# Kernel optimization log

Measured on AMD Instinct MI355X. Metric: run time of the kernel, lower is better.

The kernel has to match this reference:

```python
import jax, jax.numpy as jnp
from jax import lax
import numpy as np

WIDTH = 3.0        # tool half-width (voxels)
SIGMA = 1.0        # soft mask edge (voxels)
BLUR_SIGMA = 1.5   # post-deposit isotropic blur sigma (voxels)
EPS = 1e-8


def _gauss_blur(x, sigma):
    """Separable Gaussian blur over the last two axes of x: [B, X, Y]."""
    radius = int(3 * sigma)
    t = jnp.arange(-radius, radius + 1, dtype=x.dtype)
    k = jnp.exp(-0.5 * (t / sigma) ** 2)
    k = k / k.sum()
    x4 = x[:, None]                      # [B,1,X,Y] NCHW
    kh = k.reshape(1, 1, -1, 1)
    x4 = lax.conv_general_dilated(x4, kh, (1, 1), 'SAME')
    kw = k.reshape(1, 1, 1, -1)
    x4 = lax.conv_general_dilated(x4, kw, (1, 1), 'SAME')
    return x4[:, 0]


def setup_inputs() -> dict:
    key = jax.random.key(0)
    k1, k2, k3 = jax.random.split(key, 3)
    B, H, W = 16, 1024, 1024
    occ = jax.random.uniform(k1, (B, H, W), dtype=jnp.float32)
    # push start/end points well inside the grid (voxel coordinates)
    action_start = jax.random.uniform(k2, (B, 3), minval=200.0, maxval=800.0, dtype=jnp.float32)
    action_end = action_start + jax.random.uniform(k3, (B, 3), minval=-150.0, maxval=150.0, dtype=jnp.float32)
    return {"occ": occ, "action_start": action_start, "action_end": action_end}


def reference(occ, action_start, action_end):
    # coordinate-convention transpose (see SplatPushModel docs)
    rho = jnp.swapaxes(occ, 1, 2)            # [B, X, Y]
    B, X, Y = rho.shape
    p0 = action_start[:, :2]                 # [B,2]
    p1 = action_end[:, :2]                   # [B,2]

    d = p1 - p0
    L = jnp.sqrt(jnp.sum(d * d, axis=-1) + EPS)      # [B] segment length
    u = d / L[:, None]                               # unit push direction
    n = jnp.stack([-u[:, 1], u[:, 0]], axis=-1)      # unit normal

    gx = jnp.arange(X, dtype=rho.dtype)[None, :, None]   # [1,X,1]
    gy = jnp.arange(Y, dtype=rho.dtype)[None, None, :]   # [1,1,Y]
    bc = lambda v: v[:, None, None]                      # [B] -> [B,1,1]

    # --- swept band: soft distance-to-segment mask ---
    rx = gx - bc(p0[:, 0])
    ry = gy - bc(p0[:, 1])
    t = jnp.clip(rx * bc(u[:, 0]) + ry * bc(u[:, 1]), 0.0, L[:, None, None])
    dx = rx - t * bc(u[:, 0])
    dy = ry - t * bc(u[:, 1])
    dist = jnp.sqrt(dx * dx + dy * dy + EPS)
    swept = jax.nn.sigmoid((WIDTH - dist) / SIGMA)       # [B,X,Y]

    m_swept = jnp.sum(rho * swept, axis=(1, 2))          # [B] mass to move
    pile_depth = m_swept / (2.0 * WIDTH)                 # [B]

    # --- landing zone probe (rectangle past p1) ---
    qx = gx - bc(p1[:, 0])
    qy = gy - bc(p1[:, 1])
    s = qx * bc(u[:, 0]) + qy * bc(u[:, 1])              # along-direction coord
    r = qx * bc(n[:, 0]) + qy * bc(n[:, 1])              # perpendicular coord
    lat = jax.nn.sigmoid((WIDTH - jnp.abs(r)) / SIGMA)
    probe = jax.nn.sigmoid(s / SIGMA) * jax.nn.sigmoid((bc(pile_depth) - s) / SIGMA) * lat
    existing = jnp.sum(rho * probe, axis=(1, 2))         # [B]
    extra = existing / (2.0 * WIDTH)                     # [B] forward extension

    # --- deposit band, shifted forward by extra_depth ---
    dep_mask = (jax.nn.sigmoid((s - bc(extra)) / SIGMA)
                * jax.nn.sigmoid((bc(extra) + bc(pile_depth) - s) / SIGMA)
                * lat)
    dep_norm = m_swept / (jnp.sum(dep_mask, axis=(1, 2)) + EPS)
    dep = dep_mask * dep_norm[:, None, None]             # mass-conserving deposit

    if BLUR_SIGMA > 0:
        dep = _gauss_blur(dep, BLUR_SIGMA)

    rho_new = rho * (1.0 - swept) + dep
    return jnp.swapaxes(rho_new, 1, 2)
```

## Files before the change

kernel.cpp:

```cpp
#include <hip/hip_runtime.h>
#include <hip/hip_bf16.h>
#include <math.h>

#define BB    16
#define HH    1024
#define WW    1024
#define NPIX  (HH * WW)
#define EPSF  1e-8f
#define RAD   4
#define MARG  24.f
#define NBX   128
#define NPATCH 64

struct BlurK { float k[9]; };

__device__ __forceinline__ float sigf(float z) {
    z = fmaxf(fminf(z, 40.f), -40.f);
    return 1.f / (1.f + __expf(-z));
}

struct Geom { float p0x, p0y, p1x, p1y, L, ux, uy; };

__device__ __forceinline__ Geom load_geom(const float* as, const float* ae, int b) {
    Geom g;
    g.p0x = as[3 * b];  g.p0y = as[3 * b + 1];
    g.p1x = ae[3 * b];  g.p1y = ae[3 * b + 1];
    float dx = g.p1x - g.p0x, dy = g.p1y - g.p0y;
    g.L  = sqrtf(dx * dx + dy * dy + EPSF);
    g.ux = dx / g.L;  g.uy = dy / g.L;
    return g;
}

__device__ __forceinline__ float sweptf(const Geom& g, float x, float y) {
    float rx = x - g.p0x, ry = y - g.p0y;
    float t  = fminf(fmaxf(rx * g.ux + ry * g.uy, 0.f), g.L);
    float dx = rx - t * g.ux, dy = ry - t * g.uy;
    float dist = sqrtf(dx * dx + dy * dy + EPSF);
    return sigf(3.f - dist);
}

__device__ __forceinline__ void slat(const Geom& g, float x, float y, float& s, float& lat) {
    float qx = x - g.p1x, qy = y - g.p1y;
    s = qx * g.ux + qy * g.uy;
    float r = qx * (-g.uy) + qy * g.ux;
    lat = sigf(3.f - fabsf(r));
}

__device__ __forceinline__ void capsule_bbox(const Geom& g, float m,
                                             int& x0, int& x1, int& y0, int& y1) {
    x0 = max(0, (int)floorf(fminf(g.p0x, g.p1x) - m));
    x1 = min(WW - 1, (int)ceilf(fmaxf(g.p0x, g.p1x) + m));
    y0 = max(0, (int)floorf(fminf(g.p0y, g.p1y) - m));
    y1 = min(HH - 1, (int)ceilf(fmaxf(g.p0y, g.p1y) + m));
}

__device__ __forceinline__ void strip_bbox(const Geom& g, float s0, float s1, float m,
                                           int& x0, int& x1, int& y0, int& y1) {
    float xmin = 1e9f, xmax = -1e9f, ymin = 1e9f, ymax = -1e9f;
    #pragma unroll
    for (int i = 0; i < 4; i++) {
        float s = (i & 1) ? s1 : s0;
        float r = (i & 2) ? m : -m;
        float x = g.p1x + s * g.ux - r * g.uy;
        float y = g.p1y + s * g.uy + r * g.ux;
        xmin = fminf(xmin, x); xmax = fmaxf(xmax, x);
        ymin = fminf(ymin, y); ymax = fmaxf(ymax, y);
    }
    x0 = max(0, (int)floorf(xmin)); x1 = min(WW - 1, (int)ceilf(xmax));
    y0 = max(0, (int)floorf(ymin)); y1 = min(HH - 1, (int)ceilf(ymax));
}

__device__ __forceinline__ float brb256(float v, float* sm) {
    #pragma unroll
    for (int off = 32; off > 0; off >>= 1) v += __shfl_down(v, off);
    const int lane = threadIdx.x & 63, wid = threadIdx.x >> 6;
    if (lane == 0) sm[wid] = v;
    __syncthreads();
    float r = sm[0] + sm[1] + sm[2] + sm[3];
    __syncthreads();
    return r;
}

__global__ __launch_bounds__(256)
void k_phase1(const float* __restrict__ occ, const float* __restrict__ as,
              const float* __restrict__ ae, float* __restrict__ out,
              float* __restrict__ part1) {
    const int b = blockIdx.y, bx = blockIdx.x, tid = threadIdx.x;
    const float4* src = (const float4*)(occ + ((size_t)b << 20));
    float4*       dst = (float4*)(out + ((size_t)b << 20));
    const int cb = bx * 1024 + tid;
    float4 v0 = src[cb];
    float4 v1 = src[cb + 256];
    float4 v2 = src[cb + 512];
    float4 v3 = src[cb + 768];

    Geom g = load_geom(as, ae, b);
    int x0, x1, y0, y1; capsule_bbox(g, MARG, x0, x1, y0, y1);
    const float* base = occ + ((size_t)b << 20);
    float sum = 0.f;
    for (int y = y0 + bx; y <= y1; y += NBX) {
        float fy = (float)y;
        for (int x = x0 + tid; x <= x1; x += 256)
            sum += base[((size_t)y << 10) + x] * sweptf(g, (float)x, fy);
    }

    dst[cb] = v0; dst[cb + 256] = v1; dst[cb + 512] = v2; dst[cb + 768] = v3;

    __shared__ float sm[4];
    float bs = brb256(sum, sm);
    if (tid == 0) part1[b * NBX + bx] = bs;
}

__global__ __launch_bounds__(256)
void k_phase2(const float* __restrict__ occ, const float* __restrict__ as,
              const float* __restrict__ ae, float* __restrict__ out,
              const float* __restrict__ part1, float* __restrict__ part2) {
    const int b = blockIdx.y, bx = blockIdx.x, tid = threadIdx.x;
    const float4* src = (const float4*)(occ + ((size_t)b << 20));
    float4*       dst = (float4*)(out + ((size_t)b << 20));
    const int cb = 131072 + bx * 1024 + tid;
    float4 v0 = src[cb];
    float4 v1 = src[cb + 256];
    float4 v2 = src[cb + 512];
    float4 v3 = src[cb + 768];

    __shared__ float sm[4];
    float pv = (tid < NBX) ? part1[b * NBX + tid] : 0.f;
    const float m_swept = brb256(pv, sm);
    const float pile = m_swept * (1.f / 6.f);

    Geom g = load_geom(as, ae, b);
    int x0, x1, y0, y1; strip_bbox(g, -MARG, pile + MARG, MARG, x0, x1, y0, y1);
    const float* base = occ + ((size_t)b << 20);
    float sum = 0.f;
    for (int y = y0 + bx; y <= y1; y += NBX) {
        float fy = (float)y;
        for (int x = x0 + tid; x <= x1; x += 256) {
            float s, lat; slat(g, (float)x, fy, s, lat);
            sum += base[((size_t)y << 10) + x] * sigf(s) * sigf(pile - s) * lat;
        }
    }

    dst[cb] = v0; dst[cb + 256] = v1; dst[cb + 512] = v2; dst[cb + 768] = v3;

    float bs = brb256(sum, sm);
    if (tid == 0) part2[b * NBX + bx] = bs;
}

#define TH 8
#define TW 128
__global__ __launch_bounds__(256)
void k_final(const float* __restrict__ occ, const float* __restrict__ as,
             const float* __restrict__ ae, const float* __restrict__ part1,
             const float* __restrict__ part2, float* __restrict__ out, BlurK wk) {
    const int b = blockIdx.y, bx = blockIdx.x, tid = threadIdx.x;
    __shared__ float sm[4];
    Geom g = load_geom(as, ae, b);

    const float m_swept  = brb256((tid < NBX) ? part1[b * NBX + tid] : 0.f, sm);
    const float existing = brb256((tid < NBX) ? part2[b * NBX + tid] : 0.f, sm);
    const float pile  = m_swept * (1.f / 6.f);
    const float extra = existing * (1.f / 6.f);

    int sx0, sx1, sy0, sy1;
    strip_bbox(g, extra - MARG, extra + pile + MARG, MARG, sx0, sx1, sy0, sy1);
    float sum = 0.f;
    {
        const int w = sx1 - sx0 + 1, n = w * (sy1 - sy0 + 1);
        for (int i = tid; i < n; i += 256) {
            int y = sy0 + i / w, x = sx0 + i % w;
            float s, lat; slat(g, (float)x, (float)y, s, lat);
            sum += sigf(s - extra) * sigf(extra + pile - s) * lat;
        }
    }
    const float summask = brb256(sum, sm);
    const float dep_norm = m_swept / (summask + EPSF);

    int cx0, cx1, cy0, cy1; capsule_bbox(g, MARG, cx0, cx1, cy0, cy1);
    const int ux0 = min(cx0, sx0), ux1 = max(cx1, sx1);
    const int uy0 = min(cy0, sy0), uy1 = max(cy1, sy1);
    const int bw = ux1 - ux0 + 1, bh = uy1 - uy0 + 1;
    const int ntx = (bw + TW - 1) / TW, nty = (bh + TH - 1) / TH;

    __shared__ float draw[TH + 2 * RAD][TW + 2 * RAD];
    __shared__ float hb[TH + 2 * RAD][TW];
    const float* ob = occ + ((size_t)b << 20);
    float* outb = out + ((size_t)b << 20);

    for (int t = bx; t < ntx * nty; t += NPATCH) {
        const int tx = t % ntx, ty = t / ntx;
        const int xt = ux0 + tx * TW, yt = uy0 + ty * TH;
        for (int i = tid; i < (TH + 8) * (TW + 8); i += 256) {
            int ly = i / (TW + 8), lx = i % (TW + 8);
            int gy = yt - RAD + ly, gx = xt - RAD + lx;
            float v = 0.f;
            if (gx >= 0 && gx < WW && gy >= 0 && gy < HH) {
                float s, lat; slat(g, (float)gx, (float)gy, s, lat);
                v = sigf(s - extra) * sigf(extra + pile - s) * lat * dep_norm;
            }
            draw[ly][lx] = v;
        }
        __syncthreads();
        for (int i = tid; i < (TH + 8) * TW; i += 256) {
            int ly = i / TW, lx = i % TW;
            float acc = 0.f;
            #pragma unroll
            for (int j = 0; j < 9; j++) acc += wk.k[j] * draw[ly][lx + j];
            hb[ly][lx] = acc;
        }
        __syncthreads();
        for (int i = tid; i < TH * TW; i += 256) {
            int ly = i / TW, lx = i % TW;
            int gy = yt + ly, gx = xt + lx;
            if (gy < HH && gx < WW) {
                float acc = 0.f;
                #pragma unroll
                for (int j = 0; j < 9; j++) acc += wk.k[j] * hb[ly + j][lx];
                size_t off = ((size_t)gy << 10) + gx;
                float o = ob[off];
                outb[off] = o * (1.f - sweptf(g, (float)gx, (float)gy)) + acc;
            }
        }
        __syncthreads();
    }
}

extern "C" void kernel_launch(void* const* d_in, const int* in_sizes, int n_in,
                              void* d_out, int out_size, void* d_ws, size_t ws_size,
                              hipStream_t stream) {
    const float* occ = (const float*)d_in[0];
    const float* as  = (const float*)d_in[1];
    const float* ae  = (const float*)d_in[2];
    float* out   = (float*)d_out;
    float* part1 = (float*)d_ws;
    float* part2 = (float*)d_ws + BB * NBX;

    BlurK wk;
    {
        float s = 0.f;
        for (int i = 0; i < 9; i++) {
            float t = (float)(i - RAD) / 1.5f;
            wk.k[i] = expf(-0.5f * t * t);
            s += wk.k[i];
        }
        for (int i = 0; i < 9; i++) wk.k[i] /= s;
    }

    k_phase1<<<dim3(NBX, BB),    256, 0, stream>>>(occ, as, ae, out, part1);
    k_phase2<<<dim3(NBX, BB),    256, 0, stream>>>(occ, as, ae, out, part1, part2);
    k_final <<<dim3(NPATCH, BB), 256, 0, stream>>>(occ, as, ae, part1, part2, out, wk);
}
```

Baseline: 165.4 us.

## Fuse full copy into first pass, reuse copied data for swept sum, split summask kernel

The first kernel now copies the whole 4 MB image per batch itself, eight float4 rows per thread, and computes the swept-mass sum from those registers. This removes the second strided global read over the capsule bbox. The existing-mass kernel no longer copies and runs with 64 blocks. The deposit-mask normalisation sum moves out of the final kernel into its own grid-parallel kernel, so each patch block no longer repeats that full strip scan. This adds one more kernel launch, and the first kernel moves more bytes per block, which may lower occupancy.

```diff
diff --git a/kernel.cpp b/kernel.cpp
--- a/kernel.cpp
+++ b/kernel.cpp
@@ -9,8 +9,8 @@
 #define EPSF  1e-8f
 #define RAD   4
 #define MARG  24.f
-#define NBX   128
-#define NPATCH 64
+#define NB1   128
+#define NB2   64
 
 struct BlurK { float k[9]; };
 
@@ -82,101 +82,109 @@
 }
 
 __global__ __launch_bounds__(256)
-void k_phase1(const float* __restrict__ occ, const float* __restrict__ as,
-              const float* __restrict__ ae, float* __restrict__ out,
-              float* __restrict__ part1) {
+void k_copy_mswept(const float* __restrict__ occ, const float* __restrict__ as,
+                   const float* __restrict__ ae, float* __restrict__ out,
+                   float* __restrict__ part1) {
     const int b = blockIdx.y, bx = blockIdx.x, tid = threadIdx.x;
     const float4* src = (const float4*)(occ + ((size_t)b << 20));
     float4*       dst = (float4*)(out + ((size_t)b << 20));
-    const int cb = bx * 1024 + tid;
-    float4 v0 = src[cb];
-    float4 v1 = src[cb + 256];
-    float4 v2 = src[cb + 512];
-    float4 v3 = src[cb + 768];
-
-    Geom g = load_geom(as, ae, b);
-    int x0, x1, y0, y1; capsule_bbox(g, MARG, x0, x1, y0, y1);
-    const float* base = occ + ((size_t)b << 20);
+    const int base4 = bx * 2048 + tid;
+    float4 v[8];
+    #pragma unroll
+    for (int k = 0; k < 8; k++) v[k] = src[base4 + k * 256];
+    #pragma unroll
+    for (int k = 0; k < 8; k++) dst[base4 + k * 256] = v[k];
+
+    Geom g = load_geom(as, ae, b);
+    int cx0, cx1, cy0, cy1; capsule_bbox(g, MARG, cx0, cx1, cy0, cy1);
+    const int x = tid << 2;
     float sum = 0.f;
-    for (int y = y0 + bx; y <= y1; y += NBX) {
-        float fy = (float)y;
-        for (int x = x0 + tid; x <= x1; x += 256)
-            sum += base[((size_t)y << 10) + x] * sweptf(g, (float)x, fy);
-    }
-
-    dst[cb] = v0; dst[cb + 256] = v1; dst[cb + 512] = v2; dst[cb + 768] = v3;
-
+    if (x + 3 >= cx0 && x <= cx1) {
+        #pragma unroll
+        for (int k = 0; k < 8; k++) {
+            const int y = bx * 8 + k;
+            if (y >= cy0 && y <= cy1) {
+                float fy = (float)y, fx = (float)x;
+                sum += v[k].x * sweptf(g, fx + 0.f, fy);
+                sum += v[k].y * sweptf(g, fx + 1.f, fy);
+                sum += v[k].z * sweptf(g, fx + 2.f, fy);
+                sum += v[k].w * sweptf(g, fx + 3.f, fy);
+            }
+        }
+    }
     __shared__ float sm[4];
     float bs = brb256(sum, sm);
-    if (tid == 0) part1[b * NBX + bx] = bs;
-}
-
-__global__ __launch_bounds__(256)
-void k_phase2(const float* __restrict__ occ, const float* __restrict__ as,
-              const float* __restrict__ ae, float* __restrict__ out,
-              const float* __restrict__ part1, float* __restrict__ part2) {
-    const int b = blockIdx.y, bx = blockIdx.x, tid = threadIdx.x;
-    const float4* src = (const float4*)(occ + ((size_t)b << 20));
-    float4*       dst = (float4*)(out + ((size_t)b << 20));
-    const int cb = 131072 + bx * 1024 + tid;
-    float4 v0 = src[cb];
-    float4 v1 = src[cb + 256];
-    float4 v2 = src[cb + 512];
-    float4 v3 = src[cb + 768];
-
-    __shared__ float sm[4];
-    float pv = (tid < NBX) ? part1[b * NBX + tid] : 0.f;
-    const float m_swept = brb256(pv, sm);
+    if (tid == 0) part1[b * NB1 + bx] = bs;
+}
+
+__global__ __launch_bounds__(256)
+void k_existing(const float* __restrict__ occ, const float* __restrict__ as,
+                const float* __restrict__ ae, const float* __restrict__ part1,
+                float* __restrict__ part2) {
+    const int b = blockIdx.y, bx = blockIdx.x, tid = threadIdx.x;
+    __shared__ float sm[4];
+    const float m_swept = brb256((tid < NB1) ? part1[b * NB1 + tid] : 0.f, sm);
     const float pile = m_swept * (1.f / 6.f);
 
     Geom g = load_geom(as, ae, b);
     int x0, x1, y0, y1; strip_bbox(g, -MARG, pile + MARG, MARG, x0, x1, y0, y1);
     const float* base = occ + ((size_t)b << 20);
     float sum = 0.f;
-    for (int y = y0 + bx; y <= y1; y += NBX) {
+    for (int y = y0 + bx; y <= y1; y += NB2) {
         float fy = (float)y;
         for (int x = x0 + tid; x <= x1; x += 256) {
             float s, lat; slat(g, (float)x, fy, s, lat);
             sum += base[((size_t)y << 10) + x] * sigf(s) * sigf(pile - s) * lat;
         }
     }
-
-    dst[cb] = v0; dst[cb + 256] = v1; dst[cb + 512] = v2; dst[cb + 768] = v3;
-
     float bs = brb256(sum, sm);
-    if (tid == 0) part2[b * NBX + bx] = bs;
+    if (tid == 0) part2[b * NB2 + bx] = bs;
+}
+
+__global__ __launch_bounds__(256)
+void k_summask(const float* __restrict__ as, const float* __restrict__ ae,
+               const float* __restrict__ part1, const float* __restrict__ part2,
+               float* __restrict__ part3) {
+    const int b = blockIdx.y, bx = blockIdx.x, tid = threadIdx.x;
+    __shared__ float sm[4];
+    const float m_swept  = brb256((tid < NB1) ? part1[b * NB1 + tid] : 0.f, sm);
+    const float existing = brb256((tid < NB2) ? part2[b * NB2 + tid] : 0.f, sm);
+    const float pile  = m_swept * (1.f / 6.f);
+    const float extra = existing * (1.f / 6.f);
+
+    Geom g = load_geom(as, ae, b);
+    int x0, x1, y0, y1; strip_bbox(g, extra - MARG, extra + pile + MARG, MARG, x0, x1, y0, y1);
+    float sum = 0.f;
+    for (int y = y0 + bx; y <= y1; y += NB2) {
+        float fy = (float)y;
+        for (int x = x0 + tid; x <= x1; x += 256) {
+            float s, lat; slat(g, (float)x, fy, s, lat);
+            sum += sigf(s - extra) * sigf(extra + pile - s) * lat;
+        }
+    }
+    float bs = brb256(sum, sm);
+    if (tid == 0) part3[b * NB2 + bx] = bs;
 }
 
 #define TH 8
 #define TW 128
 __global__ __launch_bounds__(256)
-void k_final(const float* __restrict__ occ, const float* __restrict__ as,
+void k_patch(const float* __restrict__ occ, const float* __restrict__ as,
              const float* __restrict__ ae, const float* __restrict__ part1,
-             const float* __restrict__ part2, float* __restrict__ out, BlurK wk) {
-    const int b = blockIdx.y, bx = blockIdx.x, tid = threadIdx.x;
-    __shared__ float sm[4];
-    Geom g = load_geom(as, ae, b);
-
-    const float m_swept  = brb256((tid < NBX) ? part1[b * NBX + tid] : 0.f, sm);
-    const float existing = brb256((tid < NBX) ? part2[b * NBX + tid] : 0.f, sm);
-    const float pile  = m_swept * (1.f / 6.f);
-    const float extra = existing * (1.f / 6.f);
-
-    int sx0, sx1, sy0, sy1;
-    strip_bbox(g, extra - MARG, extra + pile + MARG, MARG, sx0, sx1, sy0, sy1);
-    float sum = 0.f;
-    {
-        const int w = sx1 - sx0 + 1, n = w * (sy1 - sy0 + 1);
-        for (int i = tid; i < n; i += 256) {
-            int y = sy0 + i / w, x = sx0 + i % w;
-            float s, lat; slat(g, (float)x, (float)y, s, lat);
-            sum += sigf(s - extra) * sigf(extra + pile - s) * lat;
-        }
-    }
-    const float summask = brb256(sum, sm);
+             const float* __restrict__ part2, const float* __restrict__ part3,
+             float* __restrict__ out, BlurK wk) {
+    const int b = blockIdx.y, bx = blockIdx.x, tid = threadIdx.x;
+    __shared__ float sm[4];
+    const float m_swept  = brb256((tid < NB1) ? part1[b * NB1 + tid] : 0.f, sm);
+    const float existing = brb256((tid < NB2) ? part2[b * NB2 + tid] : 0.f, sm);
+    const float summask  = brb256((tid < NB2) ? part3[b * NB2 + tid] : 0.f, sm);
+    const float pile     = m_swept * (1.f / 6.f);
+    const float extra    = existing * (1.f / 6.f);
     const float dep_norm = m_swept / (summask + EPSF);
 
+    Geom g = load_geom(as, ae, b);
     int cx0, cx1, cy0, cy1; capsule_bbox(g, MARG, cx0, cx1, cy0, cy1);
+    int sx0, sx1, sy0, sy1; strip_bbox(g, extra - MARG, extra + pile + MARG, MARG, sx0, sx1, sy0, sy1);
     const int ux0 = min(cx0, sx0), ux1 = max(cx1, sx1);
     const int uy0 = min(cy0, sy0), uy1 = max(cy1, sy1);
     const int bw = ux1 - ux0 + 1, bh = uy1 - uy0 + 1;
@@ -187,7 +195,7 @@
     const float* ob = occ + ((size_t)b << 20);
     float* outb = out + ((size_t)b << 20);
 
-    for (int t = bx; t < ntx * nty; t += NPATCH) {
+    for (int t = bx; t < ntx * nty; t += NB2) {
         const int tx = t % ntx, ty = t / ntx;
         const int xt = ux0 + tx * TW, yt = uy0 + ty * TH;
         for (int i = tid; i < (TH + 8) * (TW + 8); i += 256) {
@@ -233,7 +241,8 @@
     const float* ae  = (const float*)d_in[2];
     float* out   = (float*)d_out;
     float* part1 = (float*)d_ws;
-    float* part2 = (float*)d_ws + BB * NBX;
+    float* part2 = part1 + BB * NB1;
+    float* part3 = part2 + BB * NB2;
 
     BlurK wk;
     {
@@ -246,7 +255,8 @@
         for (int i = 0; i < 9; i++) wk.k[i] /= s;
     }
 
-    k_phase1<<<dim3(NBX, BB),    256, 0, stream>>>(occ, as, ae, out, part1);
-    k_phase2<<<dim3(NBX, BB),    256, 0, stream>>>(occ, as, ae, out, part1, part2);
-    k_final <<<dim3(NPATCH, BB), 256, 0, stream>>>(occ, as, ae, part1, part2, out, wk);
-}
+    k_copy_mswept<<<dim3(NB1, BB), 256, 0, stream>>>(occ, as, ae, out, part1);
+    k_existing   <<<dim3(NB2, BB), 256, 0, stream>>>(occ, as, ae, part1, part2);
+    k_summask    <<<dim3(NB2, BB), 256, 0, stream>>>(as, ae, part1, part2, part3);
+    k_patch      <<<dim3(NB2, BB), 256, 0, stream>>>(occ, as, ae, part1, part2, part3, out, wk);
+}
```

New measurement: 142.8 us. 13.7% less time.
